# Kernel tuning notes

Measured on AMD Instinct MI355X. Metric: run time of the kernel, lower is better.

## Reference

```python
import jax, jax.numpy as jnp
import numpy as np

D_MODEL = 1024
NUM_HEADS = 16
HEAD_DIM = D_MODEL // NUM_HEADS
B, L = 4, 4096


def _linear(x, w, b):
    # torch nn.Linear: y = x @ w.T + b, w: [out, in]
    return jnp.einsum('bld,od->blo', x, w) + b


def _elu_feature_map(x):
    return jax.nn.elu(x) + 1.0


def setup_inputs() -> dict:
    key = jax.random.key(0)
    ks = jax.random.split(key, 11)
    s = 1.0 / np.sqrt(D_MODEL)
    inp = {
        'query': jax.random.normal(ks[0], (B, L, D_MODEL), jnp.float32),
        'key': jax.random.normal(ks[1], (B, L, D_MODEL), jnp.float32),
        'value': jax.random.normal(ks[2], (B, L, D_MODEL), jnp.float32),
        'wq': jax.random.uniform(ks[3], (D_MODEL, D_MODEL), jnp.float32, -s, s),
        'bq': jax.random.uniform(ks[4], (D_MODEL,), jnp.float32, -s, s),
        'wk': jax.random.uniform(ks[5], (D_MODEL, D_MODEL), jnp.float32, -s, s),
        'bk': jax.random.uniform(ks[6], (D_MODEL,), jnp.float32, -s, s),
        'wv': jax.random.uniform(ks[7], (D_MODEL, D_MODEL), jnp.float32, -s, s),
        'bv': jax.random.uniform(ks[8], (D_MODEL,), jnp.float32, -s, s),
        'wo': jax.random.uniform(ks[9], (D_MODEL, D_MODEL), jnp.float32, -s, s),
        'bo': jax.random.uniform(ks[10], (D_MODEL,), jnp.float32, -s, s),
    }
    return inp


def reference(query, key, value, wq, bq, wk, bk, wv, bv, wo, bo):
    Bsz, Lq, _ = query.shape
    # project and split heads -> [B, H, L, hd]
    def split_heads(x):
        return x.reshape(Bsz, -1, NUM_HEADS, HEAD_DIM).transpose(0, 2, 1, 3)
    Q = split_heads(_linear(query, wq, bq))
    K = split_heads(_linear(key, wk, bk))
    V = split_heads(_linear(value, wv, bv))
    Q = _elu_feature_map(Q)
    K = _elu_feature_map(K)
    # KV: [B, H, hd, hd]
    KV = jnp.einsum('bhld,bhle->bhde', K, V)
    Ksum = K.sum(axis=2)  # [B, H, hd]
    Z = 1.0 / (jnp.einsum('bhld,bhd->bhl', Q, Ksum) + 1e-6)  # [B, H, Lq]
    out = jnp.einsum('bhld,bhde->bhle', Q, KV) * Z[..., None]
    out = out.transpose(0, 2, 1, 3).reshape(Bsz, Lq, D_MODEL)
    return _linear(out, wo, bo)
```

## Files before the change

### kernel.cpp

```cpp
#include <hip/hip_runtime.h>
#include <hip/hip_bf16.h>

typedef _Float16 half8 __attribute__((ext_vector_type(8)));
typedef _Float16 half4 __attribute__((ext_vector_type(4)));
typedef float f32x4 __attribute__((ext_vector_type(4)));

#define KDIM 1024
#define NDIM 1024
#define MROWS 16384

#define GLD_LDS16(g, l)                                                  \
  __builtin_amdgcn_global_load_lds(                                      \
      (const __attribute__((address_space(1))) void*)(g),                \
      (__attribute__((address_space(3))) void*)(l), 16, 0, 0)

__global__ __launch_bounds__(256)
void cvt_f32_to_f16(const float* __restrict__ src, _Float16* __restrict__ dst,
                    int n8) {
  for (int i = blockIdx.x * 256 + threadIdx.x; i < n8; i += gridDim.x * 256) {
    float4 f0 = ((const float4*)src)[2 * i];
    float4 f1 = ((const float4*)src)[2 * i + 1];
    half8 h;
    h[0] = (_Float16)f0.x; h[1] = (_Float16)f0.y;
    h[2] = (_Float16)f0.z; h[3] = (_Float16)f0.w;
    h[4] = (_Float16)f1.x; h[5] = (_Float16)f1.y;
    h[6] = (_Float16)f1.z; h[7] = (_Float16)f1.w;
    ((half8*)dst)[i] = h;
  }
}

template <int ACT, int TRANS, typename TOUT>
__global__ __launch_bounds__(512, 2)
void gemm_big(const _Float16* __restrict__ X, const _Float16* __restrict__ W,
              const float* __restrict__ bias, TOUT* __restrict__ Y) {
  constexpr int BM = 256, BN = 128, BK = 64;
  __shared__ _Float16 As[3 * BM * BK];
  __shared__ _Float16 Bs[3 * BN * BK];

  const int tid  = threadIdx.x;
  const int lane = tid & 63;
  const int w    = tid >> 6;
  const int wm   = w >> 1;
  const int wn   = w & 1;

  const int bid = blockIdx.x;
  const int wid = (bid & 7) * 64 + (bid >> 3);
  const int m0  = (wid >> 3) * BM;
  const int n0  = (wid & 7) * BN;

  const int lr = lane >> 3;
  const int ls = (lane & 7) ^ lr;

#define STAGE_TILE(kt, bidx)                                                  \
  {                                                                           \
    const int k0s = (kt) * BK;                                                \
    _Float16* la = As + (bidx) * (BM * BK) + w * 512;                         \
    _Float16* lb = Bs + (bidx) * (BN * BK) + w * 512;                         \
    _Pragma("unroll")                                                         \
    for (int j = 0; j < 4; ++j)                                               \
      GLD_LDS16(X + (size_t)(m0 + w * 8 + 64 * j + lr) * KDIM + k0s + ls * 8, \
                la + 4096 * j);                                               \
    _Pragma("unroll")                                                         \
    for (int j = 0; j < 2; ++j)                                               \
      GLD_LDS16(W + (size_t)(n0 + w * 8 + 64 * j + lr) * KDIM + k0s + ls * 8, \
                lb + 4096 * j);                                               \
  }

  f32x4 acc[4][4] = {};

  STAGE_TILE(0, 0);
  STAGE_TILE(1, 1);
  asm volatile("s_waitcnt vmcnt(6)" ::: "memory");
  asm volatile("s_barrier" ::: "memory");

  int bc = 0;
  for (int t = 0; t < 16; ++t) {
    int bs = bc + 2; if (bs >= 3) bs -= 3;
    const char* Ab = (const char*)As + bc * (BM * BK * 2);
    const char* Bb = (const char*)Bs + bc * (BN * BK * 2);

    half8 afr[4][2], bfr[4][2];
#pragma unroll
    for (int mi = 0; mi < 4; ++mi)
#pragma unroll
      for (int kk = 0; kk < 2; ++kk) {
        int row  = wm * 64 + mi * 16 + (lane & 15);
        int byte = row * 128 + ((lane >> 4) << 4) + kk * 64;
        byte ^= (row & 7) << 4;
        afr[mi][kk] = *(const half8*)(Ab + byte);
      }
#pragma unroll
    for (int ni = 0; ni < 4; ++ni)
#pragma unroll
      for (int kk = 0; kk < 2; ++kk) {
        int row  = wn * 64 + ni * 16 + (lane & 15);
        int byte = row * 128 + ((lane >> 4) << 4) + kk * 64;
        byte ^= (row & 7) << 4;
        bfr[ni][kk] = *(const half8*)(Bb + byte);
      }

    if (t < 14) STAGE_TILE(t + 2, bs);

    __builtin_amdgcn_s_setprio(1);
#pragma unroll
    for (int kk = 0; kk < 2; ++kk)
#pragma unroll
      for (int mi = 0; mi < 4; ++mi)
#pragma unroll
        for (int ni = 0; ni < 4; ++ni)
          acc[mi][ni] = __builtin_amdgcn_mfma_f32_16x16x32_f16(
              afr[mi][kk], bfr[ni][kk], acc[mi][ni], 0, 0, 0);
    __builtin_amdgcn_s_setprio(0);

    if (t < 15) {
      asm volatile("s_waitcnt vmcnt(6)" ::: "memory");
      asm volatile("s_barrier" ::: "memory");
    }
    ++bc; if (bc == 3) bc = 0;
  }
#undef STAGE_TILE

#pragma unroll
  for (int ni = 0; ni < 4; ++ni) {
    int col  = n0 + wn * 64 + ni * 16 + (lane & 15);
    float bv = bias[col];
#pragma unroll
    for (int mi = 0; mi < 4; ++mi) {
      int r0 = m0 + wm * 64 + mi * 16 + ((lane >> 4) << 2);
      if constexpr (TRANS) {
        int b  = r0 >> 12;
        int l0 = r0 & 4095;
        half4 hv;
#pragma unroll
        for (int i = 0; i < 4; ++i) {
          float v = acc[mi][ni][i] + bv;
          if constexpr (ACT == 1) v = (v > 0.f) ? (v + 1.f) : __expf(v);
          hv[i] = (_Float16)v;
        }
        *(half4*)((_Float16*)Y + ((size_t)(b * 1024 + col)) * 4096 + l0) = hv;
      } else {
#pragma unroll
        for (int i = 0; i < 4; ++i) {
          float v = acc[mi][ni][i] + bv;
          if constexpr (ACT == 1) v = (v > 0.f) ? (v + 1.f) : __expf(v);
          Y[(size_t)(r0 + i) * NDIM + col] = (TOUT)v;
        }
      }
    }
  }
}

__global__ __launch_bounds__(256, 2)
void kv_mfma(const _Float16* __restrict__ KT, const _Float16* __restrict__ VT,
             _Float16* __restrict__ pKV) {
  const int bh = blockIdx.x;
  const int ch = blockIdx.y;
  const int tid  = threadIdx.x;
  const int lane = tid & 63;
  const int w    = tid >> 6;

  __shared__ _Float16 As[64 * 64];
  __shared__ _Float16 Bs[64 * 64];

  const int lr = lane >> 3;
  const int ls = (lane & 7) ^ lr;
  const size_t lbase = (size_t)ch * 512 + ls * 8;
  const _Float16* gA = VT + (size_t)(bh * 64 + w * 16 + lr) * 4096 + lbase;
  const _Float16* gB = KT + (size_t)(bh * 64 + w * 16 + lr) * 4096 + lbase;
  _Float16* ldsA = As + (w * 16) * 64;
  _Float16* ldsB = Bs + (w * 16) * 64;

  half8 aones;
#pragma unroll
  for (int j = 0; j < 8; ++j) aones[j] = (lane & 15) == 0 ? (_Float16)1.0f : (_Float16)0.0f;

  f32x4 acc[5] = {};

  for (int k0 = 0; k0 < 512; k0 += 64) {
    __syncthreads();
#pragma unroll
    for (int c = 0; c < 2; ++c) {
      GLD_LDS16(gA + k0 + (size_t)(c * 8) * 4096, ldsA + c * 8 * 64);
      GLD_LDS16(gB + k0 + (size_t)(c * 8) * 4096, ldsB + c * 8 * 64);
    }
    __syncthreads();

    half8 afr[4][2], bfr[2];
#pragma unroll
    for (int m = 0; m < 4; ++m)
#pragma unroll
      for (int kk = 0; kk < 2; ++kk) {
        int row  = m * 16 + (lane & 15);
        int byte = row * 128 + ((lane >> 4) << 4) + kk * 64;
        byte ^= (row & 7) << 4;
        afr[m][kk] = *(const half8*)((const char*)As + byte);
      }
#pragma unroll
    for (int kk = 0; kk < 2; ++kk) {
      int row  = w * 16 + (lane & 15);
      int byte = row * 128 + ((lane >> 4) << 4) + kk * 64;
      byte ^= (row & 7) << 4;
      bfr[kk] = *(const half8*)((const char*)Bs + byte);
    }
#pragma unroll
    for (int kk = 0; kk < 2; ++kk) {
#pragma unroll
      for (int m = 0; m < 4; ++m)
        acc[m] = __builtin_amdgcn_mfma_f32_16x16x32_f16(afr[m][kk], bfr[kk],
                                                        acc[m], 0, 0, 0);
      acc[4] = __builtin_amdgcn_mfma_f32_16x16x32_f16(aones, bfr[kk],
                                                      acc[4], 0, 0, 0);
    }
  }

  _Float16* outp = pKV + ((size_t)ch * 64 + bh) * 5120;
  const int col = w * 16 + (lane & 15);
#pragma unroll
  for (int m = 0; m < 5; ++m) {
#pragma unroll
    for (int i = 0; i < 4; ++i) {
      int row = m * 16 + ((lane >> 4) << 2) + i;
      outp[row * 64 + col] = (_Float16)acc[m][i];
    }
  }
}

__global__ __launch_bounds__(256)
void kv_combine(const _Float16* __restrict__ pKV, _Float16* __restrict__ KVTx) {
  int g = blockIdx.x * 256 + threadIdx.x;
  int bh = g / 5120;
  int j  = g - bh * 5120;
  float s = 0.f;
#pragma unroll
  for (int ch = 0; ch < 8; ++ch)
    s += (float)pKV[((size_t)ch * 64 + bh) * 5120 + j];
  KVTx[(size_t)bh * 5120 + j] = (_Float16)s;
}

__global__ __launch_bounds__(256, 2)
void attn_kernel(const _Float16* __restrict__ Qp, const _Float16* __restrict__ KVTx,
                 _Float16* __restrict__ att) {
  const int mt = blockIdx.x;
  const int bh = blockIdx.y;
  const int b  = bh >> 4, h = bh & 15;
  const int tid = threadIdx.x;
  const int lane = tid & 63;
  const int w = tid >> 6;
  const size_t m0 = (size_t)b * 4096 + (size_t)mt * 128;

  __shared__ _Float16 As[128 * 64];
  __shared__ _Float16 Bs[80 * 64];

#pragma unroll
  for (int j = 0; j < 4; ++j) {
    int c    = tid + 256 * j;
    int row  = c >> 3;
    int col8 = (c & 7) << 3;
    int byte = row * 128 + (col8 << 1);
    byte ^= (row & 7) << 4;
    *(half8*)((char*)As + byte) =
        *(const half8*)(Qp + (m0 + row) * KDIM + h * 64 + col8);
  }
  for (int c = tid; c < 640; c += 256) {
    int row  = c >> 3;
    int col8 = (c & 7) << 3;
    int byte = row * 128 + (col8 << 1);
    byte ^= (row & 7) << 4;
    *(half8*)((char*)Bs + byte) = *(const half8*)(KVTx + (size_t)bh * 5120 + c * 8);
  }
  __syncthreads();

  f32x4 acc[2][5] = {};
  half8 afr[2][2], bfr[5][2];
#pragma unroll
  for (int m = 0; m < 2; ++m)
#pragma unroll
    for (int kk = 0; kk < 2; ++kk) {
      int row  = w * 32 + m * 16 + (lane & 15);
      int byte = row * 128 + ((lane >> 4) << 4) + kk * 64;
      byte ^= (row & 7) << 4;
      afr[m][kk] = *(const half8*)((const char*)As + byte);
    }
#pragma unroll
  for (int n = 0; n < 5; ++n)
#pragma unroll
    for (int kk = 0; kk < 2; ++kk) {
      int row  = n * 16 + (lane & 15);
      int byte = row * 128 + ((lane >> 4) << 4) + kk * 64;
      byte ^= (row & 7) << 4;
      bfr[n][kk] = *(const half8*)((const char*)Bs + byte);
    }
#pragma unroll
  for (int kk = 0; kk < 2; ++kk)
#pragma unroll
    for (int m = 0; m < 2; ++m)
#pragma unroll
      for (int n = 0; n < 5; ++n)
        acc[m][n] = __builtin_amdgcn_mfma_f32_16x16x32_f16(afr[m][kk], bfr[n][kk],
                                                           acc[m][n], 0, 0, 0);

#pragma unroll
  for (int m = 0; m < 2; ++m) {
#pragma unroll
    for (int i = 0; i < 4; ++i) {
      float dn = __shfl(acc[m][4][i], lane & 48);
      float z  = 1.f / (dn + 1e-6f);
      size_t row = m0 + w * 32 + m * 16 + ((lane >> 4) << 2) + i;
#pragma unroll
      for (int n = 0; n < 4; ++n) {
        att[row * NDIM + h * 64 + n * 16 + (lane & 15)] =
            (_Float16)(acc[m][n][i] * z);
      }
    }
  }
}

extern "C" void kernel_launch(void* const* d_in, const int* in_sizes, int n_in,
                              void* d_out, int out_size, void* d_ws, size_t ws_size,
                              hipStream_t stream) {
  const float* q  = (const float*)d_in[0];
  const float* k  = (const float*)d_in[1];
  const float* v  = (const float*)d_in[2];
  const float* wq = (const float*)d_in[3];
  const float* bq = (const float*)d_in[4];
  const float* wk = (const float*)d_in[5];
  const float* bk = (const float*)d_in[6];
  const float* wv = (const float*)d_in[7];
  const float* bv = (const float*)d_in[8];
  const float* wo = (const float*)d_in[9];
  const float* bo = (const float*)d_in[10];
  float* out = (float*)d_out;

  char* ws = (char*)d_ws;
  _Float16* Qp   = (_Float16*)(ws);
  _Float16* KT   = (_Float16*)(ws + 33554432);
  _Float16* VT   = (_Float16*)(ws + 67108864);
  _Float16* Wh   = (_Float16*)(ws + 100663296);
  _Float16* pKVh = (_Float16*)(ws + 102760448);
  _Float16* KVTx = (_Float16*)(ws + 108003328);
  _Float16* att  = KT;
  _Float16* Xh   = (_Float16*)d_out;

  const int N8_BIG = MROWS * KDIM / 8;
  const int N8_W   = KDIM * KDIM / 8;

  const int GBLK = (MROWS / 256) * (NDIM / 128);

  cvt_f32_to_f16<<<2048, 256, 0, stream>>>(q, Xh, N8_BIG);
  cvt_f32_to_f16<<<512, 256, 0, stream>>>(wq, Wh, N8_W);
  gemm_big<1, 0, _Float16><<<GBLK, 512, 0, stream>>>(Xh, Wh, bq, Qp);
  cvt_f32_to_f16<<<2048, 256, 0, stream>>>(k, Xh, N8_BIG);
  cvt_f32_to_f16<<<512, 256, 0, stream>>>(wk, Wh, N8_W);
  gemm_big<1, 1, _Float16><<<GBLK, 512, 0, stream>>>(Xh, Wh, bk, KT);
  cvt_f32_to_f16<<<2048, 256, 0, stream>>>(v, Xh, N8_BIG);
  cvt_f32_to_f16<<<512, 256, 0, stream>>>(wv, Wh, N8_W);
  gemm_big<0, 1, _Float16><<<GBLK, 512, 0, stream>>>(Xh, Wh, bv, VT);

  kv_mfma<<<dim3(64, 8), 256, 0, stream>>>(KT, VT, pKVh);
  kv_combine<<<1280, 256, 0, stream>>>(pKVh, KVTx);

  attn_kernel<<<dim3(32, 64), 256, 0, stream>>>(Qp, KVTx, att);

  cvt_f32_to_f16<<<512, 256, 0, stream>>>(wo, Wh, N8_W);
  gemm_big<0, 0, float><<<GBLK, 512, 0, stream>>>(att, Wh, bo, out);
}
```

Before: 273.4 us.

## Fuse fp32-to-fp16 conversion into GEMM tile loads via register staging

```diff
diff --git a/kernel.cpp b/kernel.cpp
--- a/kernel.cpp
+++ b/kernel.cpp
@@ -14,28 +14,13 @@
       (const __attribute__((address_space(1))) void*)(g),                \
       (__attribute__((address_space(3))) void*)(l), 16, 0, 0)
 
-__global__ __launch_bounds__(256)
-void cvt_f32_to_f16(const float* __restrict__ src, _Float16* __restrict__ dst,
-                    int n8) {
-  for (int i = blockIdx.x * 256 + threadIdx.x; i < n8; i += gridDim.x * 256) {
-    float4 f0 = ((const float4*)src)[2 * i];
-    float4 f1 = ((const float4*)src)[2 * i + 1];
-    half8 h;
-    h[0] = (_Float16)f0.x; h[1] = (_Float16)f0.y;
-    h[2] = (_Float16)f0.z; h[3] = (_Float16)f0.w;
-    h[4] = (_Float16)f1.x; h[5] = (_Float16)f1.y;
-    h[6] = (_Float16)f1.z; h[7] = (_Float16)f1.w;
-    ((half8*)dst)[i] = h;
-  }
-}
-
-template <int ACT, int TRANS, typename TOUT>
+template <int ACT, int TRANS, typename TOUT, typename TA>
 __global__ __launch_bounds__(512, 2)
-void gemm_big(const _Float16* __restrict__ X, const _Float16* __restrict__ W,
-              const float* __restrict__ bias, TOUT* __restrict__ Y) {
+void gemm_fused(const TA* __restrict__ X, const float* __restrict__ W,
+                const float* __restrict__ bias, TOUT* __restrict__ Y) {
   constexpr int BM = 256, BN = 128, BK = 64;
-  __shared__ _Float16 As[3 * BM * BK];
-  __shared__ _Float16 Bs[3 * BN * BK];
+  __shared__ _Float16 As[2 * BM * BK];
+  __shared__ _Float16 Bs[2 * BN * BK];
 
   const int tid  = threadIdx.x;
   const int lane = tid & 63;
@@ -48,37 +33,76 @@
   const int m0  = (wid >> 3) * BM;
   const int n0  = (wid & 7) * BN;
 
-  const int lr = lane >> 3;
-  const int ls = (lane & 7) ^ lr;
-
-#define STAGE_TILE(kt, bidx)                                                  \
+  const int sr = tid >> 3;
+  const int sc = (tid & 7) * 8;
+  const int wsw = (sc * 2) ^ ((sr & 7) << 4);
+
+  const TA*    Abase = X + (size_t)(m0 + sr) * KDIM + sc;
+  const float* Bbase = W + (size_t)(n0 + sr) * KDIM + sc;
+
+  float4 aR[8];
+  float4 bR[4];
+  half8  aH[4];
+  f32x4 acc[4][4] = {};
+
+#define ISSUE(T)                                                              \
   {                                                                           \
-    const int k0s = (kt) * BK;                                                \
-    _Float16* la = As + (bidx) * (BM * BK) + w * 512;                         \
-    _Float16* lb = Bs + (bidx) * (BN * BK) + w * 512;                         \
-    _Pragma("unroll")                                                         \
-    for (int j = 0; j < 4; ++j)                                               \
-      GLD_LDS16(X + (size_t)(m0 + w * 8 + 64 * j + lr) * KDIM + k0s + ls * 8, \
-                la + 4096 * j);                                               \
-    _Pragma("unroll")                                                         \
-    for (int j = 0; j < 2; ++j)                                               \
-      GLD_LDS16(W + (size_t)(n0 + w * 8 + 64 * j + lr) * KDIM + k0s + ls * 8, \
-                lb + 4096 * j);                                               \
-  }
-
-  f32x4 acc[4][4] = {};
-
-  STAGE_TILE(0, 0);
-  STAGE_TILE(1, 1);
-  asm volatile("s_waitcnt vmcnt(6)" ::: "memory");
+    const int kk0 = (T) * BK;                                                 \
+    if constexpr (sizeof(TA) == 4) {                                          \
+      _Pragma("unroll") for (int p = 0; p < 4; ++p) {                         \
+        const float* s = (const float*)Abase + (size_t)p * 64 * KDIM + kk0;   \
+        aR[2 * p]     = *(const float4*)s;                                    \
+        aR[2 * p + 1] = *(const float4*)(s + 4);                              \
+      }                                                                       \
+    } else {                                                                  \
+      _Pragma("unroll") for (int p = 0; p < 4; ++p)                           \
+        aH[p] = *(const half8*)((const _Float16*)Abase +                      \
+                                (size_t)p * 64 * KDIM + kk0);                 \
+    }                                                                         \
+    _Pragma("unroll") for (int p = 0; p < 2; ++p) {                           \
+      const float* s = Bbase + (size_t)p * 64 * KDIM + kk0;                   \
+      bR[2 * p]     = *(const float4*)s;                                      \
+      bR[2 * p + 1] = *(const float4*)(s + 4);                                \
+    }                                                                         \
+  }
+
+#define CVTWR(DB)                                                             \
+  {                                                                           \
+    _Pragma("unroll") for (int p = 0; p < 4; ++p) {                           \
+      half8 h;                                                                \
+      if constexpr (sizeof(TA) == 4) {                                        \
+        h[0] = (_Float16)aR[2 * p].x;     h[1] = (_Float16)aR[2 * p].y;       \
+        h[2] = (_Float16)aR[2 * p].z;     h[3] = (_Float16)aR[2 * p].w;       \
+        h[4] = (_Float16)aR[2 * p + 1].x; h[5] = (_Float16)aR[2 * p + 1].y;   \
+        h[6] = (_Float16)aR[2 * p + 1].z; h[7] = (_Float16)aR[2 * p + 1].w;   \
+      } else {                                                                \
+        h = aH[p];                                                            \
+      }                                                                       \
+      *(half8*)((char*)As + (DB) * 32768 + (sr + p * 64) * 128 + wsw) = h;    \
+    }                                                                         \
+    _Pragma("unroll") for (int p = 0; p < 2; ++p) {                           \
+      half8 h;                                                                \
+      h[0] = (_Float16)bR[2 * p].x;     h[1] = (_Float16)bR[2 * p].y;         \
+      h[2] = (_Float16)bR[2 * p].z;     h[3] = (_Float16)bR[2 * p].w;         \
+      h[4] = (_Float16)bR[2 * p + 1].x; h[5] = (_Float16)bR[2 * p + 1].y;     \
+      h[6] = (_Float16)bR[2 * p + 1].z; h[7] = (_Float16)bR[2 * p + 1].w;     \
+      *(half8*)((char*)Bs + (DB) * 16384 + (sr + p * 64) * 128 + wsw) = h;    \
+    }                                                                         \
+  }
+
+  ISSUE(0);
+  CVTWR(0);
+  ISSUE(1);
+  asm volatile("s_waitcnt lgkmcnt(0)" ::: "memory");
   asm volatile("s_barrier" ::: "memory");
 
-  int bc = 0;
+#pragma unroll
   for (int t = 0; t < 16; ++t) {
-    int bs = bc + 2; if (bs >= 3) bs -= 3;
-    const char* Ab = (const char*)As + bc * (BM * BK * 2);
-    const char* Bb = (const char*)Bs + bc * (BN * BK * 2);
-
+    if (t < 15) CVTWR((t + 1) & 1);
+    if (t < 14) ISSUE(t + 2);
+
+    const char* Ab = (const char*)As + (t & 1) * 32768;
+    const char* Bb = (const char*)Bs + (t & 1) * 16384;
     half8 afr[4][2], bfr[4][2];
 #pragma unroll
     for (int mi = 0; mi < 4; ++mi)
@@ -99,8 +123,6 @@
         bfr[ni][kk] = *(const half8*)(Bb + byte);
       }
 
-    if (t < 14) STAGE_TILE(t + 2, bs);
-
     __builtin_amdgcn_s_setprio(1);
 #pragma unroll
     for (int kk = 0; kk < 2; ++kk)
@@ -113,12 +135,12 @@
     __builtin_amdgcn_s_setprio(0);
 
     if (t < 15) {
-      asm volatile("s_waitcnt vmcnt(6)" ::: "memory");
+      asm volatile("s_waitcnt lgkmcnt(0)" ::: "memory");
       asm volatile("s_barrier" ::: "memory");
     }
-    ++bc; if (bc == 3) bc = 0;
-  }
-#undef STAGE_TILE
+  }
+#undef ISSUE
+#undef CVTWR
 
 #pragma unroll
   for (int ni = 0; ni < 4; ++ni) {
@@ -335,32 +357,20 @@
   _Float16* Qp   = (_Float16*)(ws);
   _Float16* KT   = (_Float16*)(ws + 33554432);
   _Float16* VT   = (_Float16*)(ws + 67108864);
-  _Float16* Wh   = (_Float16*)(ws + 100663296);
-  _Float16* pKVh = (_Float16*)(ws + 102760448);
-  _Float16* KVTx = (_Float16*)(ws + 108003328);
+  _Float16* pKVh = (_Float16*)(ws + 100663296);
+  _Float16* KVTx = (_Float16*)(ws + 105906176);
   _Float16* att  = KT;
-  _Float16* Xh   = (_Float16*)d_out;
-
-  const int N8_BIG = MROWS * KDIM / 8;
-  const int N8_W   = KDIM * KDIM / 8;
 
   const int GBLK = (MROWS / 256) * (NDIM / 128);
 
-  cvt_f32_to_f16<<<2048, 256, 0, stream>>>(q, Xh, N8_BIG);
-  cvt_f32_to_f16<<<512, 256, 0, stream>>>(wq, Wh, N8_W);
-  gemm_big<1, 0, _Float16><<<GBLK, 512, 0, stream>>>(Xh, Wh, bq, Qp);
-  cvt_f32_to_f16<<<2048, 256, 0, stream>>>(k, Xh, N8_BIG);
-  cvt_f32_to_f16<<<512, 256, 0, stream>>>(wk, Wh, N8_W);
-  gemm_big<1, 1, _Float16><<<GBLK, 512, 0, stream>>>(Xh, Wh, bk, KT);
-  cvt_f32_to_f16<<<2048, 256, 0, stream>>>(v, Xh, N8_BIG);
-  cvt_f32_to_f16<<<512, 256, 0, stream>>>(wv, Wh, N8_W);
-  gemm_big<0, 1, _Float16><<<GBLK, 512, 0, stream>>>(Xh, Wh, bv, VT);
+  gemm_fused<1, 0, _Float16, float><<<GBLK, 512, 0, stream>>>(q, wq, bq, Qp);
+  gemm_fused<1, 1, _Float16, float><<<GBLK, 512, 0, stream>>>(k, wk, bk, KT);
+  gemm_fused<0, 1, _Float16, float><<<GBLK, 512, 0, stream>>>(v, wv, bv, VT);
 
   kv_mfma<<<dim3(64, 8), 256, 0, stream>>>(KT, VT, pKVh);
   kv_combine<<<1280, 256, 0, stream>>>(pKVh, KVTx);
 
   attn_kernel<<<dim3(32, 64), 256, 0, stream>>>(Qp, KVTx, att);
 
-  cvt_f32_to_f16<<<512, 256, 0, stream>>>(wo, Wh, N8_W);
-  gemm_big<0, 0, float><<<GBLK, 512, 0, stream>>>(att, Wh, bo, out);
-}
+  gemm_fused<0, 0, float, _Float16><<<GBLK, 512, 0, stream>>>(att, wo, bo, out);
+}
```

Result: slower. 373.0 us (+36.4%).

## Fuse linear-attention apply into Q projection GEMM epilogue

Applied to the files above, without the earlier changes.

```diff
diff --git a/kernel.cpp b/kernel.cpp
--- a/kernel.cpp
+++ b/kernel.cpp
@@ -29,10 +29,11 @@
   }
 }
 
-template <int ACT, int TRANS, typename TOUT>
+template <int ACT, int TRANS, int FUSE, typename TOUT>
 __global__ __launch_bounds__(512, 2)
 void gemm_big(const _Float16* __restrict__ X, const _Float16* __restrict__ W,
-              const float* __restrict__ bias, TOUT* __restrict__ Y) {
+              const float* __restrict__ bias, TOUT* __restrict__ Y,
+              const _Float16* __restrict__ KVTx) {
   constexpr int BM = 256, BN = 128, BK = 64;
   __shared__ _Float16 As[3 * BM * BK];
   __shared__ _Float16 Bs[3 * BN * BK];
@@ -112,13 +113,91 @@
               afr[mi][kk], bfr[ni][kk], acc[mi][ni], 0, 0, 0);
     __builtin_amdgcn_s_setprio(0);
 
-    if (t < 15) {
+    if (t < 14) {
       asm volatile("s_waitcnt vmcnt(6)" ::: "memory");
       asm volatile("s_barrier" ::: "memory");
+    } else if (t == 14) {
+      asm volatile("s_waitcnt vmcnt(0)" ::: "memory");
+      asm volatile("s_barrier" ::: "memory");
     }
     ++bc; if (bc == 3) bc = 0;
   }
 #undef STAGE_TILE
+
+  if constexpr (FUSE) {
+    __syncthreads();
+    _Float16* Ct = As;
+#pragma unroll
+    for (int ni = 0; ni < 4; ++ni) {
+      int cl   = wn * 64 + ni * 16 + (lane & 15);
+      float bv = bias[n0 + cl];
+#pragma unroll
+      for (int mi = 0; mi < 4; ++mi) {
+#pragma unroll
+        for (int i = 0; i < 4; ++i) {
+          int row = wm * 64 + mi * 16 + ((lane >> 4) << 2) + i;
+          float v = acc[mi][ni][i] + bv;
+          v = (v > 0.f) ? (v + 1.f) : __expf(v);
+          int byte = row * 256 + cl * 2;
+          byte ^= (row & 7) << 4;
+          *(_Float16*)((char*)Ct + byte) = (_Float16)v;
+        }
+      }
+    }
+    _Float16* KVs = Bs;
+    const int bh0 = ((m0 >> 12) << 4) + (n0 >> 6);
+    for (int c = tid; c < 1280; c += 512) {
+      int hh  = (c >= 640) ? 1 : 0;
+      int cc  = c - hh * 640;
+      int row = cc >> 3;
+      int co8 = (cc & 7) << 3;
+      int byte = hh * 10240 + row * 128 + co8 * 2;
+      byte ^= (row & 7) << 4;
+      *(half8*)((char*)KVs + byte) =
+          *(const half8*)(KVTx + (size_t)(bh0 + hh) * 5120 + cc * 8);
+    }
+    __syncthreads();
+    f32x4 acc2[4][5] = {};
+#pragma unroll
+    for (int kk = 0; kk < 2; ++kk) {
+      half8 afr2[4], bfr2[5];
+#pragma unroll
+      for (int m = 0; m < 4; ++m) {
+        int row  = wm * 64 + m * 16 + (lane & 15);
+        int byte = row * 256 + wn * 128 + kk * 64 + ((lane >> 4) << 4);
+        byte ^= (row & 7) << 4;
+        afr2[m] = *(const half8*)((const char*)Ct + byte);
+      }
+#pragma unroll
+      for (int n = 0; n < 5; ++n) {
+        int row  = n * 16 + (lane & 15);
+        int byte = wn * 10240 + row * 128 + kk * 64 + ((lane >> 4) << 4);
+        byte ^= (row & 7) << 4;
+        bfr2[n] = *(const half8*)((const char*)KVs + byte);
+      }
+#pragma unroll
+      for (int m = 0; m < 4; ++m)
+#pragma unroll
+        for (int n = 0; n < 5; ++n)
+          acc2[m][n] = __builtin_amdgcn_mfma_f32_16x16x32_f16(
+              afr2[m], bfr2[n], acc2[m][n], 0, 0, 0);
+    }
+#pragma unroll
+    for (int m = 0; m < 4; ++m) {
+#pragma unroll
+      for (int i = 0; i < 4; ++i) {
+        float dn = __shfl(acc2[m][4][i], lane & 48);
+        float z  = 1.f / (dn + 1e-6f);
+        size_t row = (size_t)m0 + wm * 64 + m * 16 + ((lane >> 4) << 2) + i;
+#pragma unroll
+        for (int n = 0; n < 4; ++n) {
+          int col = n0 + wn * 64 + n * 16 + (lane & 15);
+          Y[row * NDIM + col] = (TOUT)(acc2[m][n][i] * z);
+        }
+      }
+    }
+    return;
+  }
 
 #pragma unroll
   for (int ni = 0; ni < 4; ++ni) {
@@ -235,84 +314,6 @@
   for (int ch = 0; ch < 8; ++ch)
     s += (float)pKV[((size_t)ch * 64 + bh) * 5120 + j];
   KVTx[(size_t)bh * 5120 + j] = (_Float16)s;
-}
-
-__global__ __launch_bounds__(256, 2)
-void attn_kernel(const _Float16* __restrict__ Qp, const _Float16* __restrict__ KVTx,
-                 _Float16* __restrict__ att) {
-  const int mt = blockIdx.x;
-  const int bh = blockIdx.y;
-  const int b  = bh >> 4, h = bh & 15;
-  const int tid = threadIdx.x;
-  const int lane = tid & 63;
-  const int w = tid >> 6;
-  const size_t m0 = (size_t)b * 4096 + (size_t)mt * 128;
-
-  __shared__ _Float16 As[128 * 64];
-  __shared__ _Float16 Bs[80 * 64];
-
-#pragma unroll
-  for (int j = 0; j < 4; ++j) {
-    int c    = tid + 256 * j;
-    int row  = c >> 3;
-    int col8 = (c & 7) << 3;
-    int byte = row * 128 + (col8 << 1);
-    byte ^= (row & 7) << 4;
-    *(half8*)((char*)As + byte) =
-        *(const half8*)(Qp + (m0 + row) * KDIM + h * 64 + col8);
-  }
-  for (int c = tid; c < 640; c += 256) {
-    int row  = c >> 3;
-    int col8 = (c & 7) << 3;
-    int byte = row * 128 + (col8 << 1);
-    byte ^= (row & 7) << 4;
-    *(half8*)((char*)Bs + byte) = *(const half8*)(KVTx + (size_t)bh * 5120 + c * 8);
-  }
-  __syncthreads();
-
-  f32x4 acc[2][5] = {};
-  half8 afr[2][2], bfr[5][2];
-#pragma unroll
-  for (int m = 0; m < 2; ++m)
-#pragma unroll
-    for (int kk = 0; kk < 2; ++kk) {
-      int row  = w * 32 + m * 16 + (lane & 15);
-      int byte = row * 128 + ((lane >> 4) << 4) + kk * 64;
-      byte ^= (row & 7) << 4;
-      afr[m][kk] = *(const half8*)((const char*)As + byte);
-    }
-#pragma unroll
-  for (int n = 0; n < 5; ++n)
-#pragma unroll
-    for (int kk = 0; kk < 2; ++kk) {
-      int row  = n * 16 + (lane & 15);
-      int byte = row * 128 + ((lane >> 4) << 4) + kk * 64;
-      byte ^= (row & 7) << 4;
-      bfr[n][kk] = *(const half8*)((const char*)Bs + byte);
-    }
-#pragma unroll
-  for (int kk = 0; kk < 2; ++kk)
-#pragma unroll
-    for (int m = 0; m < 2; ++m)
-#pragma unroll
-      for (int n = 0; n < 5; ++n)
-        acc[m][n] = __builtin_amdgcn_mfma_f32_16x16x32_f16(afr[m][kk], bfr[n][kk],
-                                                           acc[m][n], 0, 0, 0);
-
-#pragma unroll
-  for (int m = 0; m < 2; ++m) {
-#pragma unroll
-    for (int i = 0; i < 4; ++i) {
-      float dn = __shfl(acc[m][4][i], lane & 48);
-      float z  = 1.f / (dn + 1e-6f);
-      size_t row = m0 + w * 32 + m * 16 + ((lane >> 4) << 2) + i;
-#pragma unroll
-      for (int n = 0; n < 4; ++n) {
-        att[row * NDIM + h * 64 + n * 16 + (lane & 15)] =
-            (_Float16)(acc[m][n][i] * z);
-      }
-    }
-  }
 }
 
 extern "C" void kernel_launch(void* const* d_in, const int* in_sizes, int n_in,
@@ -332,7 +333,6 @@
   float* out = (float*)d_out;
 
   char* ws = (char*)d_ws;
-  _Float16* Qp   = (_Float16*)(ws);
   _Float16* KT   = (_Float16*)(ws + 33554432);
   _Float16* VT   = (_Float16*)(ws + 67108864);
   _Float16* Wh   = (_Float16*)(ws + 100663296);
@@ -346,21 +346,20 @@
 
   const int GBLK = (MROWS / 256) * (NDIM / 128);
 
+  cvt_f32_to_f16<<<2048, 256, 0, stream>>>(k, Xh, N8_BIG);
+  cvt_f32_to_f16<<<512, 256, 0, stream>>>(wk, Wh, N8_W);
+  gemm_big<1, 1, 0, _Float16><<<GBLK, 512, 0, stream>>>(Xh, Wh, bk, KT, nullptr);
+  cvt_f32_to_f16<<<2048, 256, 0, stream>>>(v, Xh, N8_BIG);
+  cvt_f32_to_f16<<<512, 256, 0, stream>>>(wv, Wh, N8_W);
+  gemm_big<0, 1, 0, _Float16><<<GBLK, 512, 0, stream>>>(Xh, Wh, bv, VT, nullptr);
+
+  kv_mfma<<<dim3(64, 8), 256, 0, stream>>>(KT, VT, pKVh);
+  kv_combine<<<1280, 256, 0, stream>>>(pKVh, KVTx);
+
   cvt_f32_to_f16<<<2048, 256, 0, stream>>>(q, Xh, N8_BIG);
   cvt_f32_to_f16<<<512, 256, 0, stream>>>(wq, Wh, N8_W);
-  gemm_big<1, 0, _Float16><<<GBLK, 512, 0, stream>>>(Xh, Wh, bq, Qp);
-  cvt_f32_to_f16<<<2048, 256, 0, stream>>>(k, Xh, N8_BIG);
-  cvt_f32_to_f16<<<512, 256, 0, stream>>>(wk, Wh, N8_W);
-  gemm_big<1, 1, _Float16><<<GBLK, 512, 0, stream>>>(Xh, Wh, bk, KT);
-  cvt_f32_to_f16<<<2048, 256, 0, stream>>>(v, Xh, N8_BIG);
-  cvt_f32_to_f16<<<512, 256, 0, stream>>>(wv, Wh, N8_W);
-  gemm_big<0, 1, _Float16><<<GBLK, 512, 0, stream>>>(Xh, Wh, bv, VT);
-
-  kv_mfma<<<dim3(64, 8), 256, 0, stream>>>(KT, VT, pKVh);
-  kv_combine<<<1280, 256, 0, stream>>>(pKVh, KVTx);
-
-  attn_kernel<<<dim3(32, 64), 256, 0, stream>>>(Qp, KVTx, att);
+  gemm_big<1, 0, 1, _Float16><<<GBLK, 512, 0, stream>>>(Xh, Wh, bq, att, KVTx);
 
   cvt_f32_to_f16<<<512, 256, 0, stream>>>(wo, Wh, N8_W);
-  gemm_big<0, 0, float><<<GBLK, 512, 0, stream>>>(att, Wh, bo, out);
-}
+  gemm_big<0, 0, 0, float><<<GBLK, 512, 0, stream>>>(att, Wh, bo, out, nullptr);
+}
```

Result: faster. 263.8 us (-3.5%).
